# Kernel tuning notes

Measured on AMD Instinct MI355X. Metric: run time of the kernel, lower is better.

## Reference

```python
import jax, jax.numpy as jnp
import numpy as np
from jax import lax

STRIDE = (1, 1)
PADDING = ((1, 1), (1, 1))  # padding=1 for 3x3 kernel -> same spatial size


def _conv_one(xi, wi, bi):
    # xi: [C_in, H, W], wi: [C_out, C_in, k, k], bi: [C_out]
    out = lax.conv_general_dilated(
        xi[None], wi, window_strides=STRIDE, padding=PADDING,
        dimension_numbers=('NCHW', 'OIHW', 'NCHW'))
    return out[0] + bi[:, None, None]


def setup_inputs() -> dict:
    key = jax.random.key(0)
    k1, k2, k3, k4 = jax.random.split(key, 4)
    B, C_in, H, W = 16, 64, 128, 128
    C_out, K, ks = 64, 5, 3
    x = jax.random.normal(k1, (B, C_in, H, W), dtype=jnp.float32)
    weights = jax.random.uniform(k2, (B, K), dtype=jnp.float32)  # attention over K kernels
    Wbank = jax.random.normal(k3, (K, C_out, C_in, ks, ks), dtype=jnp.float32)
    bbank = jax.random.normal(k4, (K, C_out), dtype=jnp.float32) * 0.1
    return {"x": x, "weights": weights, "Wbank": Wbank, "bbank": bbank}


def reference(x, weights, Wbank, bbank):
    # Per-sample aggregated kernels: [B, C_out, C_in, k, k]
    agg_w = jnp.einsum('bk,koihw->boihw', weights, Wbank)
    # Per-sample aggregated bias: [B, C_out]
    agg_b = weights @ bbank
    # Grouped conv with groups = batch, expressed as vmapped per-sample conv
    return jax.vmap(_conv_one)(x, agg_w, agg_b)
```

## Files before the change

kernel.cpp:

```cpp
#include <hip/hip_runtime.h>
#include <hip/hip_bf16.h>


typedef __attribute__((ext_vector_type(8))) __bf16 bf16x8;
typedef __attribute__((ext_vector_type(16))) float f32x16;
typedef __attribute__((ext_vector_type(4))) unsigned int u32x4;

#define NB 16
#define CI 64
#define CO 64
#define HH 128
#define WW 128
#define KBANK 5
#define ASTR 36864

__device__ __forceinline__ unsigned short f2bfu(float f) {
    __hip_bfloat16 h = __float2bfloat16(f);
    unsigned short s;
    __builtin_memcpy(&s, &h, 2);
    return s;
}

__global__ void prep_kernel(const float* __restrict__ weights,
                            const float* __restrict__ Wbank,
                            const float* __restrict__ bbank,
                            short* __restrict__ aggw,
                            float* __restrict__ aggb) {
    int idx = blockIdx.x * 256 + threadIdx.x;
    int b   = idx / ASTR;
    int rem = idx - b * ASTR;
    int j   = rem & 7;
    int co5 = (rem >> 3) & 31;
    int g   = (rem >> 8) & 1;
    int mk  = rem >> 9;
    int m   = mk / 36;
    int ks  = mk - m * 36;
    int co  = m * 32 + co5;
    int k   = ks * 16 + g * 8 + j;
    int tap = k >> 6;
    int ci  = k & 63;
    float s = 0.f;
#pragma unroll
    for (int kk = 0; kk < KBANK; ++kk)
        s += weights[b * KBANK + kk] * Wbank[((kk * CO + co) * CI + ci) * 9 + tap];
    aggw[idx] = (short)f2bfu(s);
    if (k == 0) {
        float sb = 0.f;
#pragma unroll
        for (int kk = 0; kk < KBANK; ++kk)
            sb += weights[b * KBANK + kk] * bbank[kk * CO + co];
        aggb[b * CO + co] = sb;
    }
}

__device__ __forceinline__ void load16(const float* __restrict__ xb, int r,
                                       int sw, int scg, float pv[16]) {
#pragma unroll
    for (int i = 0; i < 16; ++i)
        pv[i] = xb[((size_t)(scg * 16 + i) * HH + r) * WW + sw];
}

__device__ __forceinline__ void write16(short* __restrict__ slot, int sw, int scg,
                                        const float pv[16]) {
#pragma unroll
    for (int h = 0; h < 2; ++h) {
        unsigned u0 = (unsigned)f2bfu(pv[h * 8 + 0]) | ((unsigned)f2bfu(pv[h * 8 + 1]) << 16);
        unsigned u1 = (unsigned)f2bfu(pv[h * 8 + 2]) | ((unsigned)f2bfu(pv[h * 8 + 3]) << 16);
        unsigned u2 = (unsigned)f2bfu(pv[h * 8 + 4]) | ((unsigned)f2bfu(pv[h * 8 + 5]) << 16);
        unsigned u3 = (unsigned)f2bfu(pv[h * 8 + 6]) | ((unsigned)f2bfu(pv[h * 8 + 7]) << 16);
        *(u32x4*)&slot[((scg * 2 + h) * 130 + sw + 1) * 8] = u32x4{u0, u1, u2, u3};
    }
}

__global__ __launch_bounds__(512, 2) void conv_kernel(const float* __restrict__ x,
                                                      const short* __restrict__ aggw,
                                                      const float* __restrict__ aggb,
                                                      float* __restrict__ out) {
    __shared__ short ring[4][8][130][8];

    const int t   = threadIdx.x;
    const int lin = blockIdx.x;
    const int b     = (lin & 7) * 2 + ((lin >> 3) & 1);
    const int strip = lin >> 4;
    const int r0    = strip * 8;

    const int l  = t & 63;
    const int wv = t >> 6;
    const int m  = wv >> 2;
    const int nq = wv & 3;
    const int lm = l & 31;
    const int g  = l >> 5;

    const int sw  = t & 127;
    const int scg = t >> 7;

    const float* xb = x + (size_t)b * CI * HH * WW;
    const short* Ab = aggw + (size_t)b * ASTR + (size_t)m * 36 * 512;

    bf16x8 A[36];
#pragma unroll
    for (int ks = 0; ks < 36; ++ks)
        A[ks] = *(const bf16x8*)(Ab + ks * 512 + l * 8);

    float bias[16];
#pragma unroll
    for (int rg = 0; rg < 16; ++rg)
        bias[rg] = aggb[b * CO + m * 32 + (rg & 3) + 8 * (rg >> 2) + 4 * g];

    if (t < 64) {
        int slot = t >> 4, ch = (t >> 1) & 7, px = (t & 1) * 129;
        *(u32x4*)&ring[slot][ch][px][0] = u32x4{0u, 0u, 0u, 0u};
    }

    {
        float pv0[16] = {0,0,0,0,0,0,0,0,0,0,0,0,0,0,0,0};
        float pv1[16], pv2[16];
        if (r0 >= 1) load16(xb, r0 - 1, sw, scg, pv0);
        load16(xb, r0,     sw, scg, pv1);
        load16(xb, r0 + 1, sw, scg, pv2);
        write16(&ring[0][0][0][0], sw, scg, pv0);
        write16(&ring[1][0][0][0], sw, scg, pv1);
        write16(&ring[2][0][0][0], sw, scg, pv2);
    }
    __syncthreads();

    for (int ri = 0; ri < 8; ++ri) {
        const int r = r0 + ri;

        float pv[16] = {0,0,0,0,0,0,0,0,0,0,0,0,0,0,0,0};
        const bool stage = (ri < 7);
        if (stage && (r + 2 < 128)) load16(xb, r + 2, sw, scg, pv);

        const short* s0 = &ring[(ri    ) & 3][0][0][0];
        const short* s1 = &ring[(ri + 1) & 3][0][0][0];
        const short* s2 = &ring[(ri + 2) & 3][0][0][0];

        f32x16 acc = (f32x16)0.0f;
#pragma unroll
        for (int ks = 0; ks < 36; ++ks) {
            const int tap = ks >> 2, q = ks & 3;
            const int dy = tap / 3, dx = tap - dy * 3;
            const short* sb = (dy == 0) ? s0 : (dy == 1) ? s1 : s2;
            const int pix = nq * 32 + dx + lm;
            bf16x8 bv = *(const bf16x8*)&sb[((q * 2 + g) * 130 + pix) * 8];
            acc = __builtin_amdgcn_mfma_f32_32x32x16_bf16(A[ks], bv, acc, 0, 0, 0);
        }

        const int wc = nq * 32 + lm;
#pragma unroll
        for (int rg = 0; rg < 16; ++rg) {
            int co = m * 32 + (rg & 3) + 8 * (rg >> 2) + 4 * g;
            out[(((size_t)b * CO + co) * HH + r) * WW + wc] = acc[rg] + bias[rg];
        }

        if (stage) write16((short*)&ring[(ri + 3) & 3][0][0][0], sw, scg, pv);
        __syncthreads();
    }
}

extern "C" void kernel_launch(void* const* d_in, const int* in_sizes, int n_in,
                              void* d_out, int out_size, void* d_ws, size_t ws_size,
                              hipStream_t stream) {
    const float* x       = (const float*)d_in[0];
    const float* weights = (const float*)d_in[1];
    const float* Wbank   = (const float*)d_in[2];
    const float* bbank   = (const float*)d_in[3];
    float* out = (float*)d_out;

    short* aggw = (short*)d_ws;
    float* aggb = (float*)((char*)d_ws + 1179648);

    prep_kernel<<<dim3((NB * ASTR) / 256), dim3(256), 0, stream>>>(weights, Wbank, bbank, aggw, aggb);
    conv_kernel<<<dim3(256), dim3(512), 0, stream>>>(x, aggw, aggb, out);
}
```

Measured before the change: 40.94 us.

## Deepen input row prefetch to two rows ahead with five-slot LDS ring

Enlarges the shared-memory ring from four to five row slots and double-buffers register prefetches, so global loads for row r+3 are issued while row r is computed and stored to LDS one iteration later. The row loop is fully unrolled via compile-time indices, and __syncthreads is replaced by an explicit lgkmcnt wait, s_barrier and sched_barrier fences. The aim is to hide global load latency behind MFMA work. In exchange it uses more LDS and more registers for the second prefetch buffer, which may hurt occupancy under launch_bounds(512,2).

```diff
diff --git a/kernel.cpp b/kernel.cpp
--- a/kernel.cpp
+++ b/kernel.cpp
@@ -54,14 +54,14 @@
 }
 
 __device__ __forceinline__ void load16(const float* __restrict__ xb, int r,
-                                       int sw, int scg, float pv[16]) {
+                                       int sw, int scg, float (&pv)[16]) {
 #pragma unroll
     for (int i = 0; i < 16; ++i)
         pv[i] = xb[((size_t)(scg * 16 + i) * HH + r) * WW + sw];
 }
 
 __device__ __forceinline__ void write16(short* __restrict__ slot, int sw, int scg,
-                                        const float pv[16]) {
+                                        const float (&pv)[16]) {
 #pragma unroll
     for (int h = 0; h < 2; ++h) {
         unsigned u0 = (unsigned)f2bfu(pv[h * 8 + 0]) | ((unsigned)f2bfu(pv[h * 8 + 1]) << 16);
@@ -72,11 +72,13 @@
     }
 }
 
+template <int N> struct ic { static constexpr int v = N; };
+
 __global__ __launch_bounds__(512, 2) void conv_kernel(const float* __restrict__ x,
                                                       const short* __restrict__ aggw,
                                                       const float* __restrict__ aggb,
                                                       float* __restrict__ out) {
-    __shared__ short ring[4][8][130][8];
+    __shared__ short ring[5][8][130][8];
 
     const int t   = threadIdx.x;
     const int lin = blockIdx.x;
@@ -107,40 +109,50 @@
     for (int rg = 0; rg < 16; ++rg)
         bias[rg] = aggb[b * CO + m * 32 + (rg & 3) + 8 * (rg >> 2) + 4 * g];
 
-    if (t < 64) {
+    if (t < 80) {
         int slot = t >> 4, ch = (t >> 1) & 7, px = (t & 1) * 129;
         *(u32x4*)&ring[slot][ch][px][0] = u32x4{0u, 0u, 0u, 0u};
     }
 
+    float pvA[16], pvB[16];
     {
-        float pv0[16] = {0,0,0,0,0,0,0,0,0,0,0,0,0,0,0,0};
-        float pv1[16], pv2[16];
-        if (r0 >= 1) load16(xb, r0 - 1, sw, scg, pv0);
-        load16(xb, r0,     sw, scg, pv1);
-        load16(xb, r0 + 1, sw, scg, pv2);
-        write16(&ring[0][0][0][0], sw, scg, pv0);
-        write16(&ring[1][0][0][0], sw, scg, pv1);
-        write16(&ring[2][0][0][0], sw, scg, pv2);
+        float p0[16], p1[16], p2[16];
+        if (r0 >= 1) load16(xb, r0 - 1, sw, scg, p0);
+        else {
+#pragma unroll
+            for (int i = 0; i < 16; ++i) p0[i] = 0.f;
+        }
+        load16(xb, r0,     sw, scg, p1);
+        load16(xb, r0 + 1, sw, scg, p2);
+        write16(&ring[0][0][0][0], sw, scg, p0);
+        write16(&ring[1][0][0][0], sw, scg, p1);
+        write16(&ring[2][0][0][0], sw, scg, p2);
     }
-    __syncthreads();
+    load16(xb, r0 + 2, sw, scg, pvA);
+    asm volatile("s_waitcnt lgkmcnt(0)" ::: "memory");
+    __builtin_amdgcn_s_barrier();
+    __builtin_amdgcn_sched_barrier(0);
 
-    for (int ri = 0; ri < 8; ++ri) {
-        const int r = r0 + ri;
+    auto step = [&](auto RIc, float (&pf)[16], float (&pw)[16]) {
+        constexpr int RI = decltype(RIc)::v;
+        if (RI <= 5) {
+            if (r0 + RI + 3 < 128) {
+                load16(xb, r0 + RI + 3, sw, scg, pf);
+            } else {
+#pragma unroll
+                for (int i = 0; i < 16; ++i) pf[i] = 0.f;
+            }
+        }
+        __builtin_amdgcn_sched_barrier(0);
 
-        float pv[16] = {0,0,0,0,0,0,0,0,0,0,0,0,0,0,0,0};
-        const bool stage = (ri < 7);
-        if (stage && (r + 2 < 128)) load16(xb, r + 2, sw, scg, pv);
-
-        const short* s0 = &ring[(ri    ) & 3][0][0][0];
-        const short* s1 = &ring[(ri + 1) & 3][0][0][0];
-        const short* s2 = &ring[(ri + 2) & 3][0][0][0];
-
+        const int r = r0 + RI;
         f32x16 acc = (f32x16)0.0f;
 #pragma unroll
         for (int ks = 0; ks < 36; ++ks) {
+            constexpr int KS = 0;  (void)KS;
             const int tap = ks >> 2, q = ks & 3;
             const int dy = tap / 3, dx = tap - dy * 3;
-            const short* sb = (dy == 0) ? s0 : (dy == 1) ? s1 : s2;
+            const short* sb = &ring[(RI + (tap / 3)) % 5][0][0][0];
             const int pix = nq * 32 + dx + lm;
             bf16x8 bv = *(const bf16x8*)&sb[((q * 2 + g) * 130 + pix) * 8];
             acc = __builtin_amdgcn_mfma_f32_32x32x16_bf16(A[ks], bv, acc, 0, 0, 0);
@@ -153,9 +165,21 @@
             out[(((size_t)b * CO + co) * HH + r) * WW + wc] = acc[rg] + bias[rg];
         }
 
-        if (stage) write16((short*)&ring[(ri + 3) & 3][0][0][0], sw, scg, pv);
-        __syncthreads();
-    }
+        if (RI <= 6) write16(&ring[(RI + 3) % 5][0][0][0], sw, scg, pw);
+
+        asm volatile("s_waitcnt lgkmcnt(0)" ::: "memory");
+        __builtin_amdgcn_s_barrier();
+        __builtin_amdgcn_sched_barrier(0);
+    };
+
+    step(ic<0>{}, pvB, pvA);
+    step(ic<1>{}, pvA, pvB);
+    step(ic<2>{}, pvB, pvA);
+    step(ic<3>{}, pvA, pvB);
+    step(ic<4>{}, pvB, pvA);
+    step(ic<5>{}, pvA, pvB);
+    step(ic<6>{}, pvB, pvA);
+    step(ic<7>{}, pvA, pvB);
 }
 
 extern "C" void kernel_launch(void* const* d_in, const int* in_sizes, int n_in,
```

After: 78.58 us. 1.92x slower.

## Switch to 16x16x32 MFMA tiles, halve row strip, double grid

Applied to the files above, without the earlier changes.

Moves the conv MMA from the 32x32x16 bf16 instruction to 16x16x32, with each wave owning 16 output channels and 64 pixels over four N-tiles. This halves the per-wave A-register footprint so the launch bound can request 4 blocks per CU. The row strip per block drops from 8 to 4, which doubles the grid to 512 blocks and raises parallelism. The cost is more halo-row reloading per output row and more, smaller MFMAs.

```diff
diff --git a/kernel.cpp b/kernel.cpp
--- a/kernel.cpp
+++ b/kernel.cpp
@@ -3,7 +3,7 @@
 
 
 typedef __attribute__((ext_vector_type(8))) __bf16 bf16x8;
-typedef __attribute__((ext_vector_type(16))) float f32x16;
+typedef __attribute__((ext_vector_type(4))) float f32x4;
 typedef __attribute__((ext_vector_type(4))) unsigned int u32x4;
 
 #define NB 16
@@ -30,13 +30,12 @@
     int b   = idx / ASTR;
     int rem = idx - b * ASTR;
     int j   = rem & 7;
-    int co5 = (rem >> 3) & 31;
-    int g   = (rem >> 8) & 1;
+    int l   = (rem >> 3) & 63;
     int mk  = rem >> 9;
-    int m   = mk / 36;
-    int ks  = mk - m * 36;
-    int co  = m * 32 + co5;
-    int k   = ks * 16 + g * 8 + j;
+    int m   = mk / 18;
+    int ks  = mk - m * 18;
+    int co  = m * 16 + (l & 15);
+    int k   = ks * 32 + (l >> 4) * 8 + j;
     int tap = k >> 6;
     int ci  = k & 63;
     float s = 0.f;
@@ -54,14 +53,14 @@
 }
 
 __device__ __forceinline__ void load16(const float* __restrict__ xb, int r,
-                                       int sw, int scg, float pv[16]) {
+                                       int sw, int scg, float (&pv)[16]) {
 #pragma unroll
     for (int i = 0; i < 16; ++i)
         pv[i] = xb[((size_t)(scg * 16 + i) * HH + r) * WW + sw];
 }
 
 __device__ __forceinline__ void write16(short* __restrict__ slot, int sw, int scg,
-                                        const float pv[16]) {
+                                        const float (&pv)[16]) {
 #pragma unroll
     for (int h = 0; h < 2; ++h) {
         unsigned u0 = (unsigned)f2bfu(pv[h * 8 + 0]) | ((unsigned)f2bfu(pv[h * 8 + 1]) << 16);
@@ -72,7 +71,7 @@
     }
 }
 
-__global__ __launch_bounds__(512, 2) void conv_kernel(const float* __restrict__ x,
+__global__ __launch_bounds__(512, 4) void conv_kernel(const float* __restrict__ x,
                                                       const short* __restrict__ aggw,
                                                       const float* __restrict__ aggb,
                                                       float* __restrict__ out) {
@@ -82,30 +81,30 @@
     const int lin = blockIdx.x;
     const int b     = (lin & 7) * 2 + ((lin >> 3) & 1);
     const int strip = lin >> 4;
-    const int r0    = strip * 8;
+    const int r0    = strip * 4;
 
-    const int l  = t & 63;
-    const int wv = t >> 6;
-    const int m  = wv >> 2;
-    const int nq = wv & 3;
-    const int lm = l & 31;
-    const int g  = l >> 5;
+    const int l   = t & 63;
+    const int wv  = t >> 6;
+    const int m   = wv >> 1;
+    const int hh  = wv & 1;
+    const int ln  = l & 15;
+    const int sub = l >> 4;
 
     const int sw  = t & 127;
     const int scg = t >> 7;
 
     const float* xb = x + (size_t)b * CI * HH * WW;
-    const short* Ab = aggw + (size_t)b * ASTR + (size_t)m * 36 * 512;
+    const short* Ab = aggw + (size_t)b * ASTR + (size_t)m * 18 * 512;
 
-    bf16x8 A[36];
+    bf16x8 A[18];
 #pragma unroll
-    for (int ks = 0; ks < 36; ++ks)
+    for (int ks = 0; ks < 18; ++ks)
         A[ks] = *(const bf16x8*)(Ab + ks * 512 + l * 8);
 
-    float bias[16];
+    float bias[4];
 #pragma unroll
-    for (int rg = 0; rg < 16; ++rg)
-        bias[rg] = aggb[b * CO + m * 32 + (rg & 3) + 8 * (rg >> 2) + 4 * g];
+    for (int rg = 0; rg < 4; ++rg)
+        bias[rg] = aggb[b * CO + m * 16 + sub * 4 + rg];
 
     if (t < 64) {
         int slot = t >> 4, ch = (t >> 1) & 7, px = (t & 1) * 129;
@@ -113,47 +112,62 @@
     }
 
     {
-        float pv0[16] = {0,0,0,0,0,0,0,0,0,0,0,0,0,0,0,0};
-        float pv1[16], pv2[16];
-        if (r0 >= 1) load16(xb, r0 - 1, sw, scg, pv0);
-        load16(xb, r0,     sw, scg, pv1);
-        load16(xb, r0 + 1, sw, scg, pv2);
-        write16(&ring[0][0][0][0], sw, scg, pv0);
-        write16(&ring[1][0][0][0], sw, scg, pv1);
-        write16(&ring[2][0][0][0], sw, scg, pv2);
+        float p0[16], p1[16];
+        if (r0 >= 1) load16(xb, r0 - 1, sw, scg, p0);
+        else {
+#pragma unroll
+            for (int i = 0; i < 16; ++i) p0[i] = 0.f;
+        }
+        load16(xb, r0, sw, scg, p1);
+        write16(&ring[0][0][0][0], sw, scg, p0);
+        write16(&ring[1][0][0][0], sw, scg, p1);
+        load16(xb, r0 + 1, sw, scg, p0);
+        write16(&ring[2][0][0][0], sw, scg, p0);
     }
     __syncthreads();
 
-    for (int ri = 0; ri < 8; ++ri) {
+#pragma unroll
+    for (int ri = 0; ri < 4; ++ri) {
         const int r = r0 + ri;
 
-        float pv[16] = {0,0,0,0,0,0,0,0,0,0,0,0,0,0,0,0};
-        const bool stage = (ri < 7);
+        float pv[16];
+#pragma unroll
+        for (int i = 0; i < 16; ++i) pv[i] = 0.f;
+        const bool stage = (ri < 3);
         if (stage && (r + 2 < 128)) load16(xb, r + 2, sw, scg, pv);
 
-        const short* s0 = &ring[(ri    ) & 3][0][0][0];
-        const short* s1 = &ring[(ri + 1) & 3][0][0][0];
-        const short* s2 = &ring[(ri + 2) & 3][0][0][0];
+        f32x4 acc[4];
+#pragma unroll
+        for (int nt = 0; nt < 4; ++nt) acc[nt] = f32x4{0.f, 0.f, 0.f, 0.f};
 
-        f32x16 acc = (f32x16)0.0f;
 #pragma unroll
-        for (int ks = 0; ks < 36; ++ks) {
-            const int tap = ks >> 2, q = ks & 3;
+        for (int tap = 0; tap < 9; ++tap) {
             const int dy = tap / 3, dx = tap - dy * 3;
-            const short* sb = (dy == 0) ? s0 : (dy == 1) ? s1 : s2;
-            const int pix = nq * 32 + dx + lm;
-            bf16x8 bv = *(const bf16x8*)&sb[((q * 2 + g) * 130 + pix) * 8];
-            acc = __builtin_amdgcn_mfma_f32_32x32x16_bf16(A[ks], bv, acc, 0, 0, 0);
+            const short* sb = &ring[(ri + dy) & 3][0][0][0];
+#pragma unroll
+            for (int k2 = 0; k2 < 2; ++k2) {
+                const int ch = k2 * 4 + sub;
+#pragma unroll
+                for (int nt = 0; nt < 4; ++nt) {
+                    const int pix = hh * 64 + nt * 16 + ln + dx;
+                    bf16x8 bv = *(const bf16x8*)&sb[(ch * 130 + pix) * 8];
+                    acc[nt] = __builtin_amdgcn_mfma_f32_16x16x32_bf16(
+                        A[tap * 2 + k2], bv, acc[nt], 0, 0, 0);
+                }
+            }
         }
 
-        const int wc = nq * 32 + lm;
 #pragma unroll
-        for (int rg = 0; rg < 16; ++rg) {
-            int co = m * 32 + (rg & 3) + 8 * (rg >> 2) + 4 * g;
-            out[(((size_t)b * CO + co) * HH + r) * WW + wc] = acc[rg] + bias[rg];
+        for (int nt = 0; nt < 4; ++nt) {
+            const int wc = hh * 64 + nt * 16 + ln;
+#pragma unroll
+            for (int rg = 0; rg < 4; ++rg) {
+                int co = m * 16 + sub * 4 + rg;
+                out[(((size_t)b * CO + co) * HH + r) * WW + wc] = acc[nt][rg] + bias[rg];
+            }
         }
 
-        if (stage) write16((short*)&ring[(ri + 3) & 3][0][0][0], sw, scg, pv);
+        if (stage) write16(&ring[(ri + 3) & 3][0][0][0], sw, scg, pv);
         __syncthreads();
     }
 }
@@ -171,5 +185,5 @@
     float* aggb = (float*)((char*)d_ws + 1179648);
 
     prep_kernel<<<dim3((NB * ASTR) / 256), dim3(256), 0, stream>>>(weights, Wbank, bbank, aggw, aggb);
-    conv_kernel<<<dim3(256), dim3(512), 0, stream>>>(x, aggw, aggb, out);
+    conv_kernel<<<dim3(512), dim3(512), 0, stream>>>(x, aggw, aggb, out);
 }
```

Result: slower. 91.26 us (+122.9%).

## Stage input rows into LDS with direct global-to-LDS loads and pipelined conversion

Applied to the files above, without the earlier changes.

Replaces per-thread strided register loads of 16 channels per row with global_load_lds 16-byte transfers into an fp32 LDS double buffer. Conversion to bf16 into the ring happens from LDS. Loads for row r+3 are issued ahead of the MFMA loop and synchronised with manual vmcnt/lgkmcnt waits and raw barriers. This aims for coalesced, register-free prefetch that overlaps with compute. The cost is an extra 64 KB of LDS, which limits residency to one block per CU, and fragile hand-written wait counts.

```diff
diff --git a/kernel.cpp b/kernel.cpp
--- a/kernel.cpp
+++ b/kernel.cpp
@@ -53,36 +53,21 @@
     }
 }
 
-__device__ __forceinline__ void load16(const float* __restrict__ xb, int r,
-                                       int sw, int scg, float pv[16]) {
-#pragma unroll
-    for (int i = 0; i < 16; ++i)
-        pv[i] = xb[((size_t)(scg * 16 + i) * HH + r) * WW + sw];
-}
-
-__device__ __forceinline__ void write16(short* __restrict__ slot, int sw, int scg,
-                                        const float pv[16]) {
-#pragma unroll
-    for (int h = 0; h < 2; ++h) {
-        unsigned u0 = (unsigned)f2bfu(pv[h * 8 + 0]) | ((unsigned)f2bfu(pv[h * 8 + 1]) << 16);
-        unsigned u1 = (unsigned)f2bfu(pv[h * 8 + 2]) | ((unsigned)f2bfu(pv[h * 8 + 3]) << 16);
-        unsigned u2 = (unsigned)f2bfu(pv[h * 8 + 4]) | ((unsigned)f2bfu(pv[h * 8 + 5]) << 16);
-        unsigned u3 = (unsigned)f2bfu(pv[h * 8 + 6]) | ((unsigned)f2bfu(pv[h * 8 + 7]) << 16);
-        *(u32x4*)&slot[((scg * 2 + h) * 130 + sw + 1) * 8] = u32x4{u0, u1, u2, u3};
-    }
-}
+#define WAITV(N) asm volatile("s_waitcnt vmcnt(" #N ")" ::: "memory")
+#define WAITL0   asm volatile("s_waitcnt lgkmcnt(0)" ::: "memory")
+#define SBAR     do { __builtin_amdgcn_s_barrier(); __builtin_amdgcn_sched_barrier(0); } while (0)
 
 __global__ __launch_bounds__(512, 2) void conv_kernel(const float* __restrict__ x,
                                                       const short* __restrict__ aggw,
                                                       const float* __restrict__ aggb,
                                                       float* __restrict__ out) {
-    __shared__ short ring[4][8][130][8];
+    __shared__ short bring[4][8][130][8];
+    __shared__ float fring[2][64][128];
 
     const int t   = threadIdx.x;
     const int lin = blockIdx.x;
-    const int b     = (lin & 7) * 2 + ((lin >> 3) & 1);
-    const int strip = lin >> 4;
-    const int r0    = strip * 8;
+    const int b   = (lin & 7) * 2 + ((lin >> 3) & 1);
+    const int r0  = (lin >> 4) * 8;
 
     const int l  = t & 63;
     const int wv = t >> 6;
@@ -90,9 +75,6 @@
     const int nq = wv & 3;
     const int lm = l & 31;
     const int g  = l >> 5;
-
-    const int sw  = t & 127;
-    const int scg = t >> 7;
 
     const float* xb = x + (size_t)b * CI * HH * WW;
     const short* Ab = aggw + (size_t)b * ASTR + (size_t)m * 36 * 512;
@@ -109,38 +91,73 @@
 
     if (t < 64) {
         int slot = t >> 4, ch = (t >> 1) & 7, px = (t & 1) * 129;
-        *(u32x4*)&ring[slot][ch][px][0] = u32x4{0u, 0u, 0u, 0u};
+        *(u32x4*)&bring[slot][ch][px][0] = u32x4{0u, 0u, 0u, 0u};
     }
 
-    {
-        float pv0[16] = {0,0,0,0,0,0,0,0,0,0,0,0,0,0,0,0};
-        float pv1[16], pv2[16];
-        if (r0 >= 1) load16(xb, r0 - 1, sw, scg, pv0);
-        load16(xb, r0,     sw, scg, pv1);
-        load16(xb, r0 + 1, sw, scg, pv2);
-        write16(&ring[0][0][0][0], sw, scg, pv0);
-        write16(&ring[1][0][0][0], sw, scg, pv1);
-        write16(&ring[2][0][0][0], sw, scg, pv2);
-    }
-    __syncthreads();
+    auto stage = [&](int r, int fs) {
+        float* fbase = &fring[fs][0][0];
+#pragma unroll
+        for (int i = 0; i < 4; ++i) {
+            int c  = i * 512 + t;
+            int ci = c >> 5;
+            int w  = (c & 31) * 4;
+            const float* src = xb + ((size_t)ci * HH + r) * WW + w;
+            float* dst = fbase + (size_t)(i * 512 + (t & ~63)) * 4;
+            __builtin_amdgcn_global_load_lds(
+                (const __attribute__((address_space(1))) void*)src,
+                (__attribute__((address_space(3))) void*)dst, 16, 0, 0);
+        }
+    };
 
-    for (int ri = 0; ri < 8; ++ri) {
-        const int r = r0 + ri;
+    auto convertz = [&](const float* fbase, int bs, bool zero) {
+#pragma unroll
+        for (int k2 = 0; k2 < 2; ++k2) {
+            int c   = k2 * 512 + t;
+            int ch  = c >> 7;
+            int pix = (c & 127) + 1;
+            unsigned u0 = 0, u1 = 0, u2 = 0, u3 = 0;
+            if (!zero) {
+                const float* p = fbase + ch * 1024 + (pix - 1);
+                u0 = (unsigned)f2bfu(p[0])   | ((unsigned)f2bfu(p[128]) << 16);
+                u1 = (unsigned)f2bfu(p[256]) | ((unsigned)f2bfu(p[384]) << 16);
+                u2 = (unsigned)f2bfu(p[512]) | ((unsigned)f2bfu(p[640]) << 16);
+                u3 = (unsigned)f2bfu(p[768]) | ((unsigned)f2bfu(p[896]) << 16);
+            }
+            *(u32x4*)&bring[bs][ch][pix][0] = u32x4{u0, u1, u2, u3};
+        }
+    };
 
-        float pv[16] = {0,0,0,0,0,0,0,0,0,0,0,0,0,0,0,0};
-        const bool stage = (ri < 7);
-        if (stage && (r + 2 < 128)) load16(xb, r + 2, sw, scg, pv);
+    if (r0 > 0) stage(r0 - 1, 0);
+    stage(r0, 1);
+    WAITV(4); SBAR;
+    if (r0 > 0) convertz(&fring[0][0][0], 0, false);
+    else        convertz(nullptr,         0, true);
+    WAITL0; SBAR;
+    stage(r0 + 1, 0);
+    WAITV(4); SBAR;
+    convertz(&fring[1][0][0], 1, false);
+    WAITL0; SBAR;
+    stage(r0 + 2, 1);
+    WAITV(4); SBAR;
+    convertz(&fring[0][0][0], 2, false);
+    WAITV(0);
+    WAITL0; SBAR;
 
-        const short* s0 = &ring[(ri    ) & 3][0][0][0];
-        const short* s1 = &ring[(ri + 1) & 3][0][0][0];
-        const short* s2 = &ring[(ri + 2) & 3][0][0][0];
+#pragma unroll
+    for (int s = 0; s < 8; ++s) {
+        const int r = r0 + s;
+
+        if (r + 2 <= 127) convertz(&fring[(s + 1) & 1][0][0], (s + 3) & 3, false);
+        else              convertz(nullptr,                   (s + 3) & 3, true);
+
+        if (r + 3 <= 127) stage(r + 3, s & 1);
 
         f32x16 acc = (f32x16)0.0f;
 #pragma unroll
         for (int ks = 0; ks < 36; ++ks) {
             const int tap = ks >> 2, q = ks & 3;
             const int dy = tap / 3, dx = tap - dy * 3;
-            const short* sb = (dy == 0) ? s0 : (dy == 1) ? s1 : s2;
+            const short* sb = &bring[(s + dy) & 3][0][0][0];
             const int pix = nq * 32 + dx + lm;
             bf16x8 bv = *(const bf16x8*)&sb[((q * 2 + g) * 130 + pix) * 8];
             acc = __builtin_amdgcn_mfma_f32_32x32x16_bf16(A[ks], bv, acc, 0, 0, 0);
@@ -153,8 +170,9 @@
             out[(((size_t)b * CO + co) * HH + r) * WW + wc] = acc[rg] + bias[rg];
         }
 
-        if (stage) write16((short*)&ring[(ri + 3) & 3][0][0][0], sw, scg, pv);
-        __syncthreads();
+        WAITV(16);
+        WAITL0;
+        SBAR;
     }
 }
 
```

Measured after the change: 40.24 us. About the same (-1.7%).
